# Kernel optimization log

Hardware: AMD Instinct MI355X
Metric: run time of the kernel (lower is better)

The kernel has to match this reference:

```python
import jax, jax.numpy as jnp
import numpy as np

N = 128
MAX_LEN = 1024
L = 1024
BATCH = 32


def _legs_transition(n):
    # HiPPO-LegS A, B matrices (float64 numpy, matches torch module's transition())
    q = np.arange(n, dtype=np.float64)
    col, row = np.meshgrid(q, q)
    r = 2 * q + 1
    M = -(np.where(row >= col, r, 0) - np.diag(q))
    T = np.sqrt(np.diag(2 * q + 1))
    A = T @ M @ np.linalg.inv(T)
    B = np.diag(T)
    return A, B


def _stacked_bilinear(n, max_length):
    # Bilinear discretization per timestep t: (I - A/(2t))^{-1} (I + A/(2t)), (I - A/(2t))^{-1} B/t
    A, B = _legs_transition(n)
    t = np.arange(1, max_length + 1, dtype=np.float64)[:, None, None]  # (L,1,1)
    I = np.eye(n)
    At = A[None] / t                                   # (L,N,N)
    lhs = I - At / 2
    A_st = np.linalg.solve(lhs, I + At / 2)            # (L,N,N)
    Bt = (B[None, :] / t[:, 0, 0][:, None])[..., None]  # (L,N,1)
    B_st = np.linalg.solve(lhs, Bt)[..., 0]            # (L,N)
    return A_st.astype(np.float32), B_st.astype(np.float32)


def setup_inputs() -> dict:
    key = jax.random.key(0)
    inputs = jax.random.normal(key, (L, BATCH), dtype=jnp.float32)
    A_st, B_st = _stacked_bilinear(N, MAX_LEN)
    return {
        "inputs": inputs,
        "A_stacked": jnp.asarray(A_st),
        "B_stacked": jnp.asarray(B_st),
    }


def reference(inputs, A_stacked, B_stacked):
    # inputs: (L, B); A_stacked: (L, N, N); B_stacked: (L, N)
    Lc = inputs.shape[0]
    u = inputs[..., None] * B_stacked[:Lc, None, :]  # (L, B, N)

    def step(s, Au):
        A_t, u_t = Au                                 # (N,N), (B,N)
        s = jnp.einsum("ij,bj->bi", A_t, s) + u_t
        return s, s

    s0 = jnp.zeros_like(u[0])
    _, xs = jax.lax.scan(step, s0, (A_stacked[:Lc], u))
    return xs  # (L, B, N)
```

## Files before the change

kernel.cpp:

```cpp
#include <hip/hip_runtime.h>


#define LDK 136
#define PKF 11264

using f16 = _Float16;
typedef __attribute__((ext_vector_type(8))) f16 f16x8;
typedef __attribute__((ext_vector_type(4))) float f32x4;

__device__ __forceinline__ f32x4 mfma3(f16x8 ah, f16x8 al, f16x8 bh, f16x8 bl,
                                       f32x4 c) {
  c = __builtin_amdgcn_mfma_f32_16x16x32_f16(ah, bh, c, 0, 0, 0);
  c = __builtin_amdgcn_mfma_f32_16x16x32_f16(ah, bl, c, 0, 0, 0);
  c = __builtin_amdgcn_mfma_f32_16x16x32_f16(al, bh, c, 0, 0, 0);
  return c;
}

__device__ __forceinline__ void split8(const float* v, f16x8& h, f16x8& l) {
#pragma unroll
  for (int j = 0; j < 8; ++j) {
    const float x = v[j];
    const f16 hh = (f16)x;
    h[j] = hh;
    l[j] = (f16)(x - (float)hh);
  }
}

__device__ __forceinline__ int slot2mt(int h, int slot) {
  if (h == 0) return (slot & 1) ? 7 - (slot >> 1) : (slot >> 1);
  return (slot & 1) ? 5 - (slot >> 1) : 2 + (slot >> 1);
}

__device__ __forceinline__ void gload_lds16(const float* g, float* l) {
  __builtin_amdgcn_global_load_lds(
      (const __attribute__((address_space(1))) unsigned int*)g,
      (__attribute__((address_space(3))) unsigned int*)l, 16, 0, 0);
}


__device__ __forceinline__ int pk_src_off(int m) {
  int b, local, ccm1, sh;
  if (m < 128)      { b = 0; local = m;       ccm1 = 3;  sh = 2; }
  else if (m < 384) { b = 1; local = m - 128; ccm1 = 7;  sh = 3; }
  else if (m < 896) { b = 2; local = m - 384; ccm1 = 15; sh = 4; }
  else              { b = 3; local = m - 896; ccm1 = 15; sh = 4; }
  const int ri = local >> sh, cp = local & ccm1;
  const int c = cp ^ (ri & ccm1);
  return (b * 32 + ri) * 128 + c * 8;
}

__device__ __forceinline__ void read_pk(const f16* __restrict__ Bs, int nt,
                                        int lr, int j0, f16x8& v) {
  const int b = nt >> 1;
  const int ri = ((nt & 1) << 4) + lr;
  const int ccm1 = (b == 0) ? 3 : (b == 1) ? 7 : 15;
  const int fb = (b == 0) ? 0 : (b == 1) ? 1024 : (b == 2) ? 3072 : 7168;
  const int c = j0 ^ (ri & ccm1);
  v = *(const f16x8*)(Bs + fb + ri * ((ccm1 + 1) * 8) + c * 8);
}

template <int NT, int IT>
__device__ __forceinline__ void pk_precompute(int tid, int (&src)[IT]) {
#pragma unroll
  for (int it = 0; it < IT; ++it) {
    const int m = tid + it * NT;
    src[it] = (m < 1408) ? pk_src_off(m) : 0;
  }
}

template <int NT, int IT>
__device__ __forceinline__ void pk_stage(const f16* __restrict__ gMh,
                                         const f16* __restrict__ gMl,
                                         f16* __restrict__ dH,
                                         f16* __restrict__ dL,
                                         const int (&src)[IT], int tid) {
#pragma unroll
  for (int it = 0; it < IT; ++it) {
    const int m = tid + it * NT;
    if (it < IT - 1 || m < 1408) {
      gload_lds16((const float*)(gMh + src[it]), (float*)(dH + m * 8));
      gload_lds16((const float*)(gMl + src[it]), (float*)(dL + m * 8));
    }
  }
}

__device__ __forceinline__ void compute_soff(int tid, int (&soff)[8]) {
#pragma unroll
  for (int it = 0; it < 8; ++it) {
    const int m = tid + it * 320;
    if (m < 2304) {
      const int kt = (m >= 768) + (m >= 1536) + (m >= 2048);
      const int local = m - ((kt >= 1) * 768 + (kt >= 2) * 768 + (kt >= 3) * 512);
      const int rp = local >> 3, c = local & 7;
      const int r = rp + 32 + (kt >= 2) * 32 + (kt >= 3) * 32;
      soff[it] = r * 128 + kt * 32 + ((c ^ (rp & 7)) << 2);
    } else {
      soff[it] = 0;
    }
  }
}

__device__ __forceinline__ void issue_A(const float* __restrict__ Al,
                                        float* __restrict__ Ast,
                                        const int (&soff)[8], int tid) {
#pragma unroll
  for (int it = 0; it < 8; ++it) {
    if (it < 7 || tid < 64)
      gload_lds16(Al + soff[it], Ast + (tid + it * 320) * 4);
  }
}

__device__ __forceinline__ void read_staged(const float* __restrict__ Ast,
                                            int nt, int kt, int lr, int q,
                                            f16x8& ch, f16x8& cl) {
  const int rp = nt * 16 + lr - (32 + (kt >= 2) * 32 + (kt >= 3) * 32);
  const float* pb =
      Ast + ((kt >= 1) * 3072 + (kt >= 2) * 3072 + (kt >= 3) * 2048) + rp * 32;
  float raw[8];
  *(float4*)&raw[0] = *(const float4*)(pb + (((2 * q + 0) ^ (rp & 7)) << 2));
  *(float4*)&raw[4] = *(const float4*)(pb + (((2 * q + 1) ^ (rp & 7)) << 2));
  split8(raw, ch, cl);
}

__device__ __forceinline__ void chain_step_pk(
    const f16* __restrict__ Bsh, const f16* __restrict__ Bsl,
    const float* __restrict__ aux0, f16* __restrict__ Ph, f16* __restrict__ Pl,
    int wv, int mt, const f16* __restrict__ nMh, const f16* __restrict__ nMl,
    f16* __restrict__ stH, f16* __restrict__ stL, const int (&src)[5],
    int tid) {
  const int lane = tid & 63;
  const int lr = lane & 15, q = lane >> 4;
  const bool wrow = (mt >= 8);
  const int ktA0 = wrow ? 0 : (mt >> 1);
  f16x8 ah[4], al[4];
#pragma unroll
  for (int kt = 0; kt < 4; ++kt) {
    if (kt >= ktA0) {
      const int off = (wv * 16 + lr) * LDK + kt * 32 + q * 8;
      ah[kt] = *(const f16x8*)(Ph + off);
      al[kt] = *(const f16x8*)(Pl + off);
    }
  }
  f32x4 acc[8];
#pragma unroll
  for (int nt = 0; nt < 8; ++nt) acc[nt] = (f32x4){0.f, 0.f, 0.f, 0.f};
#pragma unroll
  for (int nt = 0; nt < 8; ++nt) {
    if (wrow || nt >= mt) {
#pragma unroll
      for (int kt = 0; kt < 4; ++kt) {
        if (kt >= ktA0 && kt <= (nt >> 1)) {
          f16x8 bh, bl;
          const int j0 = kt * 4 + q;
          read_pk(Bsh, nt, lr, j0, bh);
          read_pk(Bsl, nt, lr, j0, bl);
          acc[nt] = mfma3(ah[kt], al[kt], bh, bl, acc[nt]);
        }
      }
    }
  }
  __syncthreads();
  if (nMh) pk_stage<320, 5>(nMh, nMl, stH, stL, src, tid);
#pragma unroll
  for (int nt = 0; nt < 8; ++nt) {
    if (!(wrow || nt >= mt)) continue;
    float v[4] = {acc[nt][0], acc[nt][1], acc[nt][2], acc[nt][3]};
    if (wrow) {
      const int b0 = (mt - 8) * 16 + q * 4;
      const float4 w4 = *(const float4*)(aux0 + (nt * 16 + lr) * 32 + b0);
      v[0] += w4.x; v[1] += w4.y; v[2] += w4.z; v[3] += w4.w;
    }
#pragma unroll
    for (int r = 0; r < 4; ++r) {
      const int o = (wv * 16 + q * 4 + r) * LDK + nt * 16 + lr;
      const f16 hh = (f16)v[r];
      Ph[o] = hh;
      Pl[o] = (f16)(v[r] - (float)hh);
    }
  }
  __syncthreads();
}

__device__ __forceinline__ void chain_step_k1(const float* __restrict__ Acur,
                                              const float* __restrict__ Anext,
                                              const float* __restrict__ x32,
                                              const float* __restrict__ Bvl,
                                              f16* __restrict__ Ph,
                                              f16* __restrict__ Pl,
                                              float* __restrict__ Ast,
                                              const int (&soff)[8],
                                              int wv, int mt) {
  const int tid = threadIdx.x;
  const int lane = tid & 63, lr = lane & 15, q = lane >> 4;
  const bool wrow = (mt >= 8);
  const int ktA0 = wrow ? 0 : (mt >> 1);
  f16x8 ah[4], al[4];
#pragma unroll
  for (int kt = 0; kt < 4; ++kt) {
    if (kt >= ktA0) {
      const int off = (wv * 16 + lr) * LDK + kt * 32 + q * 8;
      ah[kt] = *(const f16x8*)(Ph + off);
      al[kt] = *(const f16x8*)(Pl + off);
    }
  }
  const bool need0 = wrow || mt == 0;
  const bool need1 = wrow || mt <= 1;
  float dir0[8], dir1[8];
  if (need0) {
    const float* p = Acur + lr * 128 + q * 8;
    *(float4*)&dir0[0] = *(const float4*)p;
    *(float4*)&dir0[4] = *(const float4*)(p + 4);
  }
  if (need1) {
    const float* p = Acur + (16 + lr) * 128 + q * 8;
    *(float4*)&dir1[0] = *(const float4*)p;
    *(float4*)&dir1[4] = *(const float4*)(p + 4);
  }
  f32x4 acc[8];
#pragma unroll
  for (int nt = 0; nt < 8; ++nt) acc[nt] = (f32x4){0.f, 0.f, 0.f, 0.f};
#pragma unroll
  for (int nt = 2; nt < 8; ++nt) {
    if (wrow || nt >= mt) {
#pragma unroll
      for (int kt = 0; kt < 4; ++kt) {
        if (kt >= ktA0 && kt <= (nt >> 1)) {
          f16x8 ch, cl;
          read_staged(Ast, nt, kt, lr, q, ch, cl);
          acc[nt] = mfma3(ah[kt], al[kt], ch, cl, acc[nt]);
        }
      }
    }
  }
  if (need0) {
    f16x8 ch, cl;
    split8(dir0, ch, cl);
    acc[0] = mfma3(ah[0], al[0], ch, cl, acc[0]);
  }
  if (need1) {
    f16x8 ch, cl;
    split8(dir1, ch, cl);
    acc[1] = mfma3(ah[0], al[0], ch, cl, acc[1]);
  }
  __syncthreads();
  if (Anext) issue_A(Anext, Ast, soff, tid);
#pragma unroll
  for (int nt = 0; nt < 8; ++nt) {
    if (!(wrow || nt >= mt)) continue;
    float v[4] = {acc[nt][0], acc[nt][1], acc[nt][2], acc[nt][3]};
    if (wrow) {
      const int b0 = (mt - 8) * 16 + q * 4;
      const float4 x4 = *(const float4*)(x32 + b0);
      const float bn = Bvl[nt * 16 + lr];
      v[0] += bn * x4.x; v[1] += bn * x4.y; v[2] += bn * x4.z; v[3] += bn * x4.w;
    }
#pragma unroll
    for (int r = 0; r < 4; ++r) {
      const int o = (wv * 16 + q * 4 + r) * LDK + nt * 16 + lr;
      const f16 hh = (f16)v[r];
      Ph[o] = hh;
      Pl[o] = (f16)(v[r] - (float)hh);
    }
  }
  __syncthreads();
}

__device__ __forceinline__ void chain_copyout(const f16* __restrict__ Ph,
                                              const f16* __restrict__ Pl, int h,
                                              f16* __restrict__ oMh,
                                              f16* __restrict__ oMl,
                                              float* __restrict__ oW) {
  const int tid = threadIdx.x;
  for (int t = tid; t < 1024; t += 320) {
    const int i = t >> 3;
    const int slot = (t >> 1) & 3;
    const int half = t & 1;
    const int mtg = slot2mt(h, slot);
    const int y0 = mtg * 16 + half * 8;
    if ((y0 >> 5) > (i >> 5)) continue;
    f16x8 hv, lv;
#pragma unroll
    for (int e = 0; e < 8; ++e) {
      hv[e] = Ph[(slot * 16 + half * 8 + e) * LDK + i];
      lv[e] = Pl[(slot * 16 + half * 8 + e) * LDK + i];
    }
    *(f16x8*)(oMh + i * 128 + y0) = hv;
    *(f16x8*)(oMl + i * 128 + y0) = lv;
  }
  for (int t = tid; t < 512; t += 320) {
    const int n = t >> 2, b4 = (t & 3) * 4;
    float4 o;
    float* po = (float*)&o;
#pragma unroll
    for (int e = 0; e < 4; ++e)
      po[e] = (float)Ph[(64 + b4 + e) * LDK + n] + (float)Pl[(64 + b4 + e) * LDK + n];
    *(float4*)(oW + n * 32 + h * 16 + b4) = o;
  }
}

__device__ __forceinline__ void load_prev_to_P(const f16* pMh, const f16* pMl,
                                               const float* pW, int h,
                                               f16* Ph, f16* Pl) {
  const int tid = threadIdx.x;
  for (int t = tid; t < 1024; t += 320) {
    const int k = t >> 3, u = t & 7;
    const int slot = u >> 1, half = u & 1;
    const int mtg = slot2mt(h, slot);
    const int y0 = mtg * 16 + half * 8;
    f16x8 hv, lv;
    if ((y0 >> 5) <= (k >> 5)) {
      hv = *(const f16x8*)(pMh + k * 128 + y0);
      lv = *(const f16x8*)(pMl + k * 128 + y0);
    } else {
#pragma unroll
      for (int e = 0; e < 8; ++e) { hv[e] = (f16)0.f; lv[e] = (f16)0.f; }
    }
#pragma unroll
    for (int e = 0; e < 8; ++e) {
      Ph[(slot * 16 + half * 8 + e) * LDK + k] = hv[e];
      Pl[(slot * 16 + half * 8 + e) * LDK + k] = lv[e];
    }
  }
  for (int t = tid; t < 2048; t += 320) {
    const int n = t >> 4, b = t & 15;
    const float wv0 = pW[n * 32 + h * 16 + b];
    const f16 hh = (f16)wv0;
    Ph[(64 + b) * LDK + n] = hh;
    Pl[(64 + b) * LDK + n] = (f16)(wv0 - (float)hh);
  }
  __syncthreads();
}

__device__ __forceinline__ void state_step_h_b16(const f16* __restrict__ Bh16,
                                                 const f16* __restrict__ Bl16,
                                                 const float* __restrict__ aux0,
                                                 f16* __restrict__ Sh,
                                                 f16* __restrict__ Sl, int h) {
  const int tid = threadIdx.x;
  const int wv4 = tid >> 6;
  const bool act = (wv4 < 4);
  const int wv = wv4 & 3;
  const int lane = tid & 63, lr = lane & 15, q = lane >> 4;
  const int nts[2] = {wv, 7 - wv};
  const int ktAmax = (7 - wv) >> 1;
  f16x8 ah[4], al[4];
  f16x8 bh[2][4], bl[2][4];
  f32x4 acc[2];
  if (act) {
#pragma unroll
    for (int kt = 0; kt < 4; ++kt)
      if (kt <= ktAmax) {
        const int off = lr * LDK + kt * 32 + q * 8;
        ah[kt] = *(const f16x8*)(Sh + off);
        al[kt] = *(const f16x8*)(Sl + off);
      }
#pragma unroll
    for (int ni = 0; ni < 2; ++ni) {
      const int nt = nts[ni];
#pragma unroll
      for (int kt = 0; kt < 4; ++kt)
        if (kt <= (nt >> 1)) {
          const int o = (nt * 16 + lr) * 128 + kt * 32 + q * 8;
          bh[ni][kt] = *(const f16x8*)(Bh16 + o);
          bl[ni][kt] = *(const f16x8*)(Bl16 + o);
        }
    }
#pragma unroll
    for (int ni = 0; ni < 2; ++ni) acc[ni] = (f32x4){0.f, 0.f, 0.f, 0.f};
#pragma unroll
    for (int ni = 0; ni < 2; ++ni) {
      const int nt = nts[ni];
#pragma unroll
      for (int kt = 0; kt < 4; ++kt)
        if (kt <= (nt >> 1))
          acc[ni] = mfma3(ah[kt], al[kt], bh[ni][kt], bl[ni][kt], acc[ni]);
    }
  }
  __syncthreads();
  if (act) {
#pragma unroll
    for (int ni = 0; ni < 2; ++ni) {
      const int nt = nts[ni];
      float v[4] = {acc[ni][0], acc[ni][1], acc[ni][2], acc[ni][3]};
      const int bq = q * 4;
      const float4 w4 = *(const float4*)(aux0 + (nt * 16 + lr) * 32 + h * 16 + bq);
      v[0] += w4.x; v[1] += w4.y; v[2] += w4.z; v[3] += w4.w;
#pragma unroll
      for (int r = 0; r < 4; ++r) {
        const int o = (bq + r) * LDK + nt * 16 + lr;
        const f16 hh = (f16)v[r];
        Sh[o] = hh;
        Sl[o] = (f16)(v[r] - (float)hh);
      }
    }
  }
  __syncthreads();
}

__device__ __forceinline__ void state_step_pk(
    const f16* __restrict__ Bsh, const f16* __restrict__ Bsl,
    const float* __restrict__ aux0, f16* __restrict__ Sh,
    f16* __restrict__ Sl, int h, const f16* __restrict__ nMh,
    const f16* __restrict__ nMl, f16* __restrict__ stH,
    f16* __restrict__ stL, const int (&src)[6], int tid) {
  const int wv = (tid >> 6) & 3;
  const int lane = tid & 63, lr = lane & 15, q = lane >> 4;
  const int nts[2] = {wv, 7 - wv};
  const int ktAmax = (7 - wv) >> 1;
  f16x8 ah[4], al[4];
#pragma unroll
  for (int kt = 0; kt < 4; ++kt)
    if (kt <= ktAmax) {
      const int off = lr * LDK + kt * 32 + q * 8;
      ah[kt] = *(const f16x8*)(Sh + off);
      al[kt] = *(const f16x8*)(Sl + off);
    }
  f32x4 acc[2];
#pragma unroll
  for (int ni = 0; ni < 2; ++ni) acc[ni] = (f32x4){0.f, 0.f, 0.f, 0.f};
#pragma unroll
  for (int ni = 0; ni < 2; ++ni) {
    const int nt = nts[ni];
#pragma unroll
    for (int kt = 0; kt < 4; ++kt)
      if (kt <= (nt >> 1)) {
        f16x8 bh, bl;
        const int j0 = kt * 4 + q;
        read_pk(Bsh, nt, lr, j0, bh);
        read_pk(Bsl, nt, lr, j0, bl);
        acc[ni] = mfma3(ah[kt], al[kt], bh, bl, acc[ni]);
      }
  }
  __syncthreads();
  if (nMh) pk_stage<256, 6>(nMh, nMl, stH, stL, src, tid);
#pragma unroll
  for (int ni = 0; ni < 2; ++ni) {
    const int nt = nts[ni];
    float v[4] = {acc[ni][0], acc[ni][1], acc[ni][2], acc[ni][3]};
    const int bq = q * 4;
    const float4 w4 = *(const float4*)(aux0 + (nt * 16 + lr) * 32 + h * 16 + bq);
    v[0] += w4.x; v[1] += w4.y; v[2] += w4.z; v[3] += w4.w;
#pragma unroll
    for (int r = 0; r < 4; ++r) {
      const int o = (bq + r) * LDK + nt * 16 + lr;
      const f16 hh = (f16)v[r];
      Sh[o] = hh;
      Sl[o] = (f16)(v[r] - (float)hh);
    }
  }
  __syncthreads();
}

__device__ __forceinline__ void state_step_h_staged(
    const float* __restrict__ Acur, const float* __restrict__ Anext,
    const float* __restrict__ x32, const float* __restrict__ Bvl,
    f16* __restrict__ Sh, f16* __restrict__ Sl, float* __restrict__ outp,
    int h, float* __restrict__ Ast, const int (&soff)[8]) {
  const int tid = threadIdx.x;
  const int wv4 = tid >> 6;
  const bool act = (wv4 < 4);
  const int wv = wv4 & 3;
  const int lane = tid & 63, lr = lane & 15, q = lane >> 4;
  const int ntL = wv, ntH = 7 - wv;
  f32x4 accL = (f32x4){0.f, 0.f, 0.f, 0.f}, accH = accL;
  if (act) {
    const int ktAmax = ntH >> 1;
    f16x8 ah[4], al[4];
#pragma unroll
    for (int kt = 0; kt < 4; ++kt)
      if (kt <= ktAmax) {
        const int off = lr * LDK + kt * 32 + q * 8;
        ah[kt] = *(const f16x8*)(Sh + off);
        al[kt] = *(const f16x8*)(Sl + off);
      }
    float dir[8];
    if (wv < 2) {
      const float* p = Acur + (ntL * 16 + lr) * 128 + q * 8;
      *(float4*)&dir[0] = *(const float4*)p;
      *(float4*)&dir[4] = *(const float4*)(p + 4);
    }
#pragma unroll
    for (int kt = 0; kt < 4; ++kt) {
      if (kt <= (ntH >> 1)) {
        f16x8 ch, cl;
        read_staged(Ast, ntH, kt, lr, q, ch, cl);
        accH = mfma3(ah[kt], al[kt], ch, cl, accH);
      }
    }
    if (wv >= 2) {
#pragma unroll
      for (int kt = 0; kt < 4; ++kt) {
        if (kt <= (ntL >> 1)) {
          f16x8 ch, cl;
          read_staged(Ast, ntL, kt, lr, q, ch, cl);
          accL = mfma3(ah[kt], al[kt], ch, cl, accL);
        }
      }
    } else {
      f16x8 ch, cl;
      split8(dir, ch, cl);
      accL = mfma3(ah[0], al[0], ch, cl, accL);
    }
  }
  __syncthreads();
  if (Anext) issue_A(Anext, Ast, soff, tid);
  if (act) {
#pragma unroll
    for (int ni = 0; ni < 2; ++ni) {
      const int nt = (ni == 0) ? ntL : ntH;
      const f32x4 a = (ni == 0) ? accL : accH;
      float v[4] = {a[0], a[1], a[2], a[3]};
      const int bq = q * 4;
      const float4 x4 = *(const float4*)(x32 + h * 16 + bq);
      const float bn = Bvl[nt * 16 + lr];
      v[0] += bn * x4.x; v[1] += bn * x4.y; v[2] += bn * x4.z; v[3] += bn * x4.w;
      if (outp) {
#pragma unroll
        for (int r = 0; r < 4; ++r)
          outp[(h * 16 + bq + r) * 128 + nt * 16 + lr] = v[r];
      }
#pragma unroll
      for (int r = 0; r < 4; ++r) {
        const int o = (bq + r) * LDK + nt * 16 + lr;
        const f16 hh = (f16)v[r];
        Sh[o] = hh;
        Sl[o] = (f16)(v[r] - (float)hh);
      }
    }
  }
  __syncthreads();
}

__global__ __launch_bounds__(320) void k1_chunks(const float* __restrict__ A,
                                                 const float* __restrict__ x,
                                                 const float* __restrict__ Bv,
                                                 f16* __restrict__ Mh,
                                                 f16* __restrict__ Ml,
                                                 float* __restrict__ Wf) {
  __shared__ f16 Ph[80 * LDK], Pl[80 * LDK];
  __shared__ float Ast[9216];
  const int tid = threadIdx.x;
  const int c = blockIdx.x >> 1, h = blockIdx.x & 1;
  const int l0 = 4 * c;
  int soff[8];
  compute_soff(tid, soff);
  issue_A(A + (size_t)(l0 + 1) * 16384, Ast, soff, tid);
  const float* A0 = A + (size_t)l0 * 16384;
  for (int t = tid; t < 2048; t += 320) {
    const int k = t >> 4, u = t & 15;
    const int slot = u >> 2, fo = (u & 3) * 4;
    const int mtg = slot2mt(h, slot);
    const int y = mtg * 16 + fo;
    float vv[4];
    if ((y >> 5) <= (k >> 5)) {
      const float4 v = *(const float4*)(A0 + k * 128 + y);
      vv[0] = v.x; vv[1] = v.y; vv[2] = v.z; vv[3] = v.w;
    } else {
      vv[0] = vv[1] = vv[2] = vv[3] = 0.f;
    }
#pragma unroll
    for (int e = 0; e < 4; ++e) {
      const f16 hh = (f16)vv[e];
      Ph[(slot * 16 + fo + e) * LDK + k] = hh;
      Pl[(slot * 16 + fo + e) * LDK + k] = (f16)(vv[e] - (float)hh);
    }
  }
  for (int t = tid; t < 512; t += 320) {
    const int b = t >> 5, n4 = (t & 31) * 4;
    const float xb = x[l0 * 32 + h * 16 + b];
#pragma unroll
    for (int e = 0; e < 4; ++e) {
      const float u = xb * Bv[l0 * 128 + n4 + e];
      const f16 hh = (f16)u;
      Ph[(64 + b) * LDK + n4 + e] = hh;
      Pl[(64 + b) * LDK + n4 + e] = (f16)(u - (float)hh);
    }
  }
  __syncthreads();
  const int wv = tid >> 6;
  const int mt = (wv == 4) ? (8 + h) : slot2mt(h, wv);
  chain_step_k1(A + (size_t)(l0 + 1) * 16384, A + (size_t)(l0 + 2) * 16384,
                x + (l0 + 1) * 32, Bv + (l0 + 1) * 128, Ph, Pl, Ast, soff, wv, mt);
  chain_step_k1(A + (size_t)(l0 + 2) * 16384, A + (size_t)(l0 + 3) * 16384,
                x + (l0 + 2) * 32, Bv + (l0 + 2) * 128, Ph, Pl, Ast, soff, wv, mt);
  chain_step_k1(A + (size_t)(l0 + 3) * 16384, nullptr,
                x + (l0 + 3) * 32, Bv + (l0 + 3) * 128, Ph, Pl, Ast, soff, wv, mt);
  chain_copyout(Ph, Pl, h, Mh + (size_t)c * 16384, Ml + (size_t)c * 16384,
                Wf + (size_t)c * 4096);
}

__global__ __launch_bounds__(320) void mscan(const f16* __restrict__ MhA,
                                             const f16* __restrict__ MlA,
                                             const float* __restrict__ WA,
                                             f16* __restrict__ MhB,
                                             f16* __restrict__ MlB,
                                             float* __restrict__ WB) {
  __shared__ f16 Ph[80 * LDK], Pl[80 * LDK];
  __shared__ f16 BstH[2][PKF], BstL[2][PKF];
  const int g = blockIdx.x >> 1, h = blockIdx.x & 1;
  const int tid = threadIdx.x;
  int src[5];
  pk_precompute<320, 5>(tid, src);
  const size_t n0 = (size_t)(16 * g);
  pk_stage<320, 5>(MhA + (n0 + 1) * 16384, MlA + (n0 + 1) * 16384,
                   BstH[1], BstL[1], src, tid);
  load_prev_to_P(MhA + n0 * 16384, MlA + n0 * 16384, WA + n0 * 4096, h, Ph, Pl);
  const int wv = tid >> 6;
  const int mt = (wv == 4) ? (8 + h) : slot2mt(h, wv);
#pragma unroll 1
  for (int j = 1; j <= 15; ++j) {
    const size_t nd = n0 + j;
    const int cur = j & 1;
    const bool more = (j < 15);
    chain_step_pk(BstH[cur], BstL[cur], WA + nd * 4096, Ph, Pl, wv, mt,
                  more ? MhA + (nd + 1) * 16384 : nullptr,
                  more ? MlA + (nd + 1) * 16384 : nullptr,
                  BstH[cur ^ 1], BstL[cur ^ 1], src, tid);
    chain_copyout(Ph, Pl, h, MhB + nd * 16384, MlB + nd * 16384,
                  WB + nd * 4096);
  }
}

__global__ __launch_bounds__(256) void gscan(const f16* __restrict__ MhB,
                                             const f16* __restrict__ MlB,
                                             const float* __restrict__ WB,
                                             float* __restrict__ Ef) {
  __shared__ f16 Sh[16 * LDK], Sl[16 * LDK];
  __shared__ f16 GstH[2][PKF], GstL[2][PKF];
  const int g = blockIdx.x >> 1, h = blockIdx.x & 1;
  const int tid = threadIdx.x;
  int src[6];
  pk_precompute<256, 6>(tid, src);
  for (int t = tid; t < 16 * LDK; t += 256) { Sh[t] = (f16)0.f; Sl[t] = (f16)0.f; }
  if (g > 0)
    pk_stage<256, 6>(MhB + (size_t)15 * 16384, MlB + (size_t)15 * 16384,
                     GstH[0], GstL[0], src, tid);
  __syncthreads();
#pragma unroll 1
  for (int t = 0; t < g; ++t) {
    const size_t nd = (size_t)(16 * t + 15);
    const size_t nn = (size_t)(16 * (t + 1) + 15);
    const int cur = t & 1;
    const bool more = (t + 1 < g);
    state_step_pk(GstH[cur], GstL[cur], WB + nd * 4096, Sh, Sl, h,
                  more ? MhB + nn * 16384 : nullptr,
                  more ? MlB + nn * 16384 : nullptr,
                  GstH[cur ^ 1], GstL[cur ^ 1], src, tid);
  }
  for (int t = tid; t < 2048; t += 256) {
    const int row = t & 15, n = t >> 4;
    Ef[(size_t)g * 4096 + n * 32 + h * 16 + row] =
        (float)Sh[row * LDK + n] + (float)Sl[row * LDK + n];
  }
}

__global__ __launch_bounds__(320) void k3h(const float* __restrict__ A,
                                           const float* __restrict__ x,
                                           const float* __restrict__ Bv,
                                           const f16* __restrict__ MhA,
                                           const f16* __restrict__ MlA,
                                           const float* __restrict__ WA,
                                           const f16* __restrict__ MhB,
                                           const f16* __restrict__ MlB,
                                           const float* __restrict__ WB,
                                           const float* __restrict__ Ef,
                                           float* __restrict__ out) {
  __shared__ f16 Sh[16 * LDK], Sl[16 * LDK];
  __shared__ float Ast[9216];
  const int tid = threadIdx.x;
  const int c = blockIdx.x >> 1, h = blockIdx.x & 1;
  const int g = c >> 4, j = c & 15;
  int soff[8];
  compute_soff(tid, soff);
  issue_A(A + (size_t)(4 * c) * 16384, Ast, soff, tid);
  const float* Ew = Ef + (size_t)g * 4096;
  for (int tt = tid; tt < 2048; tt += 320) {
    const int row = tt & 15, n = tt >> 4;
    const float v = Ew[n * 32 + h * 16 + row];
    const f16 hh = (f16)v;
    Sh[row * LDK + n] = hh;
    Sl[row * LDK + n] = (f16)(v - (float)hh);
  }
  __syncthreads();
  if (j > 0) {
    const int nd = c - 1, jp = j - 1;
    const bool inA = (jp == 0);
    const f16* mh = (inA ? MhA : MhB) + (size_t)nd * 16384;
    const f16* ml = (inA ? MlA : MlB) + (size_t)nd * 16384;
    const float* w = (inA ? WA : WB) + (size_t)nd * 4096;
    state_step_h_b16(mh, ml, w, Sh, Sl, h);
  }
#pragma unroll 1
  for (int t4 = 0; t4 < 4; ++t4) {
    const int l = 4 * c + t4;
    const float* Anext = (t4 < 3) ? A + (size_t)(l + 1) * 16384 : nullptr;
    state_step_h_staged(A + (size_t)l * 16384, Anext, x + l * 32, Bv + l * 128,
                        Sh, Sl, out + (size_t)l * 4096, h, Ast, soff);
  }
}

extern "C" void kernel_launch(void* const* d_in, const int* in_sizes, int n_in,
                              void* d_out, int out_size, void* d_ws, size_t ws_size,
                              hipStream_t stream) {
  const float* x  = (const float*)d_in[0];
  const float* A  = (const float*)d_in[1];
  const float* Bv = (const float*)d_in[2];
  float* out = (float*)d_out;

  f16* MhA = (f16*)d_ws;
  f16* MlA = MhA + 256 * 16384;
  float* WA = (float*)(MlA + 256 * 16384);
  f16* MhB = (f16*)(WA + 256 * 4096);
  f16* MlB = MhB + 256 * 16384;
  float* WB = (float*)(MlB + 256 * 16384);
  float* Ef = WB + 256 * 4096;

  k1_chunks<<<512, 320, 0, stream>>>(A, x, Bv, MhA, MlA, WA);
  mscan<<<32, 320, 0, stream>>>(MhA, MlA, WA, MhB, MlB, WB);
  gscan<<<32, 256, 0, stream>>>(MhB, MlB, WB, Ef);
  k3h<<<512, 320, 0, stream>>>(A, x, Bv, MhA, MlA, WA, MhB, MlB, WB, Ef, out);
}
```

Before: 292.2 us.

## Split mscan work across twice as many smaller blocks and write outputs directly

The chunk-prefix matrix scan kernel now runs as 64 blocks of 192 threads instead of 32 blocks of 320. Each block handles half of the row slots, and only one half-block carries the W row. Results are written straight from accumulators to global memory, which drops the separate copy-out pass and one barrier per step. Prefetch staging is issued at the start of each step in both mscan and gscan rather than after a mid-step barrier. This spreads a serial, latency-bound phase over more CUs, at the cost of loading the shared B staging matrices twice and leaving some waves idle.

```diff
diff --git a/kernel.cpp b/kernel.cpp
--- a/kernel.cpp
+++ b/kernel.cpp
@@ -6,6 +6,7 @@
 
 using f16 = _Float16;
 typedef __attribute__((ext_vector_type(8))) f16 f16x8;
+typedef __attribute__((ext_vector_type(4))) f16 f16x4;
 typedef __attribute__((ext_vector_type(4))) float f32x4;
 
 __device__ __forceinline__ f32x4 mfma3(f16x8 ah, f16x8 al, f16x8 bh, f16x8 bl,
@@ -77,7 +78,7 @@
 #pragma unroll
   for (int it = 0; it < IT; ++it) {
     const int m = tid + it * NT;
-    if (it < IT - 1 || m < 1408) {
+    if (m < 1408) {
       gload_lds16((const float*)(gMh + src[it]), (float*)(dH + m * 8));
       gload_lds16((const float*)(gMl + src[it]), (float*)(dL + m * 8));
     }
@@ -120,65 +121,6 @@
   *(float4*)&raw[0] = *(const float4*)(pb + (((2 * q + 0) ^ (rp & 7)) << 2));
   *(float4*)&raw[4] = *(const float4*)(pb + (((2 * q + 1) ^ (rp & 7)) << 2));
   split8(raw, ch, cl);
-}
-
-__device__ __forceinline__ void chain_step_pk(
-    const f16* __restrict__ Bsh, const f16* __restrict__ Bsl,
-    const float* __restrict__ aux0, f16* __restrict__ Ph, f16* __restrict__ Pl,
-    int wv, int mt, const f16* __restrict__ nMh, const f16* __restrict__ nMl,
-    f16* __restrict__ stH, f16* __restrict__ stL, const int (&src)[5],
-    int tid) {
-  const int lane = tid & 63;
-  const int lr = lane & 15, q = lane >> 4;
-  const bool wrow = (mt >= 8);
-  const int ktA0 = wrow ? 0 : (mt >> 1);
-  f16x8 ah[4], al[4];
-#pragma unroll
-  for (int kt = 0; kt < 4; ++kt) {
-    if (kt >= ktA0) {
-      const int off = (wv * 16 + lr) * LDK + kt * 32 + q * 8;
-      ah[kt] = *(const f16x8*)(Ph + off);
-      al[kt] = *(const f16x8*)(Pl + off);
-    }
-  }
-  f32x4 acc[8];
-#pragma unroll
-  for (int nt = 0; nt < 8; ++nt) acc[nt] = (f32x4){0.f, 0.f, 0.f, 0.f};
-#pragma unroll
-  for (int nt = 0; nt < 8; ++nt) {
-    if (wrow || nt >= mt) {
-#pragma unroll
-      for (int kt = 0; kt < 4; ++kt) {
-        if (kt >= ktA0 && kt <= (nt >> 1)) {
-          f16x8 bh, bl;
-          const int j0 = kt * 4 + q;
-          read_pk(Bsh, nt, lr, j0, bh);
-          read_pk(Bsl, nt, lr, j0, bl);
-          acc[nt] = mfma3(ah[kt], al[kt], bh, bl, acc[nt]);
-        }
-      }
-    }
-  }
-  __syncthreads();
-  if (nMh) pk_stage<320, 5>(nMh, nMl, stH, stL, src, tid);
-#pragma unroll
-  for (int nt = 0; nt < 8; ++nt) {
-    if (!(wrow || nt >= mt)) continue;
-    float v[4] = {acc[nt][0], acc[nt][1], acc[nt][2], acc[nt][3]};
-    if (wrow) {
-      const int b0 = (mt - 8) * 16 + q * 4;
-      const float4 w4 = *(const float4*)(aux0 + (nt * 16 + lr) * 32 + b0);
-      v[0] += w4.x; v[1] += w4.y; v[2] += w4.z; v[3] += w4.w;
-    }
-#pragma unroll
-    for (int r = 0; r < 4; ++r) {
-      const int o = (wv * 16 + q * 4 + r) * LDK + nt * 16 + lr;
-      const f16 hh = (f16)v[r];
-      Ph[o] = hh;
-      Pl[o] = (f16)(v[r] - (float)hh);
-    }
-  }
-  __syncthreads();
 }
 
 __device__ __forceinline__ void chain_step_k1(const float* __restrict__ Acur,
@@ -296,39 +238,6 @@
       po[e] = (float)Ph[(64 + b4 + e) * LDK + n] + (float)Pl[(64 + b4 + e) * LDK + n];
     *(float4*)(oW + n * 32 + h * 16 + b4) = o;
   }
-}
-
-__device__ __forceinline__ void load_prev_to_P(const f16* pMh, const f16* pMl,
-                                               const float* pW, int h,
-                                               f16* Ph, f16* Pl) {
-  const int tid = threadIdx.x;
-  for (int t = tid; t < 1024; t += 320) {
-    const int k = t >> 3, u = t & 7;
-    const int slot = u >> 1, half = u & 1;
-    const int mtg = slot2mt(h, slot);
-    const int y0 = mtg * 16 + half * 8;
-    f16x8 hv, lv;
-    if ((y0 >> 5) <= (k >> 5)) {
-      hv = *(const f16x8*)(pMh + k * 128 + y0);
-      lv = *(const f16x8*)(pMl + k * 128 + y0);
-    } else {
-#pragma unroll
-      for (int e = 0; e < 8; ++e) { hv[e] = (f16)0.f; lv[e] = (f16)0.f; }
-    }
-#pragma unroll
-    for (int e = 0; e < 8; ++e) {
-      Ph[(slot * 16 + half * 8 + e) * LDK + k] = hv[e];
-      Pl[(slot * 16 + half * 8 + e) * LDK + k] = lv[e];
-    }
-  }
-  for (int t = tid; t < 2048; t += 320) {
-    const int n = t >> 4, b = t & 15;
-    const float wv0 = pW[n * 32 + h * 16 + b];
-    const f16 hh = (f16)wv0;
-    Ph[(64 + b) * LDK + n] = hh;
-    Pl[(64 + b) * LDK + n] = (f16)(wv0 - (float)hh);
-  }
-  __syncthreads();
 }
 
 __device__ __forceinline__ void state_step_h_b16(const f16* __restrict__ Bh16,
@@ -392,60 +301,6 @@
         Sh[o] = hh;
         Sl[o] = (f16)(v[r] - (float)hh);
       }
-    }
-  }
-  __syncthreads();
-}
-
-__device__ __forceinline__ void state_step_pk(
-    const f16* __restrict__ Bsh, const f16* __restrict__ Bsl,
-    const float* __restrict__ aux0, f16* __restrict__ Sh,
-    f16* __restrict__ Sl, int h, const f16* __restrict__ nMh,
-    const f16* __restrict__ nMl, f16* __restrict__ stH,
-    f16* __restrict__ stL, const int (&src)[6], int tid) {
-  const int wv = (tid >> 6) & 3;
-  const int lane = tid & 63, lr = lane & 15, q = lane >> 4;
-  const int nts[2] = {wv, 7 - wv};
-  const int ktAmax = (7 - wv) >> 1;
-  f16x8 ah[4], al[4];
-#pragma unroll
-  for (int kt = 0; kt < 4; ++kt)
-    if (kt <= ktAmax) {
-      const int off = lr * LDK + kt * 32 + q * 8;
-      ah[kt] = *(const f16x8*)(Sh + off);
-      al[kt] = *(const f16x8*)(Sl + off);
-    }
-  f32x4 acc[2];
-#pragma unroll
-  for (int ni = 0; ni < 2; ++ni) acc[ni] = (f32x4){0.f, 0.f, 0.f, 0.f};
-#pragma unroll
-  for (int ni = 0; ni < 2; ++ni) {
-    const int nt = nts[ni];
-#pragma unroll
-    for (int kt = 0; kt < 4; ++kt)
-      if (kt <= (nt >> 1)) {
-        f16x8 bh, bl;
-        const int j0 = kt * 4 + q;
-        read_pk(Bsh, nt, lr, j0, bh);
-        read_pk(Bsl, nt, lr, j0, bl);
-        acc[ni] = mfma3(ah[kt], al[kt], bh, bl, acc[ni]);
-      }
-  }
-  __syncthreads();
-  if (nMh) pk_stage<256, 6>(nMh, nMl, stH, stL, src, tid);
-#pragma unroll
-  for (int ni = 0; ni < 2; ++ni) {
-    const int nt = nts[ni];
-    float v[4] = {acc[ni][0], acc[ni][1], acc[ni][2], acc[ni][3]};
-    const int bq = q * 4;
-    const float4 w4 = *(const float4*)(aux0 + (nt * 16 + lr) * 32 + h * 16 + bq);
-    v[0] += w4.x; v[1] += w4.y; v[2] += w4.z; v[3] += w4.w;
-#pragma unroll
-    for (int r = 0; r < 4; ++r) {
-      const int o = (bq + r) * LDK + nt * 16 + lr;
-      const f16 hh = (f16)v[r];
-      Sh[o] = hh;
-      Sl[o] = (f16)(v[r] - (float)hh);
     }
   }
   __syncthreads();
@@ -589,35 +444,161 @@
                 Wf + (size_t)c * 4096);
 }
 
-__global__ __launch_bounds__(320) void mscan(const f16* __restrict__ MhA,
-                                             const f16* __restrict__ MlA,
-                                             const float* __restrict__ WA,
-                                             f16* __restrict__ MhB,
-                                             f16* __restrict__ MlB,
-                                             float* __restrict__ WB) {
-  __shared__ f16 Ph[80 * LDK], Pl[80 * LDK];
+__global__ __launch_bounds__(192) void mscan_s(const f16* __restrict__ MhA,
+                                               const f16* __restrict__ MlA,
+                                               const float* __restrict__ WA,
+                                               f16* __restrict__ MhB,
+                                               f16* __restrict__ MlB,
+                                               float* __restrict__ WB) {
+  __shared__ f16 Ph[48 * LDK], Pl[48 * LDK];
   __shared__ f16 BstH[2][PKF], BstL[2][PKF];
-  const int g = blockIdx.x >> 1, h = blockIdx.x & 1;
+  const int bid = blockIdx.x;
+  const int g = bid >> 2, h = (bid >> 1) & 1, half = bid & 1;
   const int tid = threadIdx.x;
-  int src[5];
-  pk_precompute<320, 5>(tid, src);
+  const int wv = tid >> 6;
+  const int lane = tid & 63, lr = lane & 15, q = lane >> 4;
+  const bool isW = (half == 0 && wv == 2);
+  const bool isM = (wv < 2);
+  const int mt = isW ? (8 + h) : (isM ? slot2mt(h, half * 2 + wv) : 0);
+  const int lw = wv * 16;
+  const int ktA0 = isW ? 0 : (mt >> 1);
   const size_t n0 = (size_t)(16 * g);
-  pk_stage<320, 5>(MhA + (n0 + 1) * 16384, MlA + (n0 + 1) * 16384,
+
+  int src[8];
+  pk_precompute<192, 8>(tid, src);
+  pk_stage<192, 8>(MhA + (n0 + 1) * 16384, MlA + (n0 + 1) * 16384,
                    BstH[1], BstL[1], src, tid);
-  load_prev_to_P(MhA + n0 * 16384, MlA + n0 * 16384, WA + n0 * 4096, h, Ph, Pl);
-  const int wv = tid >> 6;
-  const int mt = (wv == 4) ? (8 + h) : slot2mt(h, wv);
+  if (isM) {
+    const f16* pMh = MhA + n0 * 16384;
+    const f16* pMl = MlA + n0 * 16384;
+#pragma unroll
+    for (int it = 0; it < 4; ++it) {
+      const int t = lane + it * 64;
+      const int k = t >> 1, hk = t & 1;
+      const int y0 = mt * 16 + hk * 8;
+      f16x8 hv, lv;
+      if ((y0 >> 5) <= (k >> 5)) {
+        hv = *(const f16x8*)(pMh + k * 128 + y0);
+        lv = *(const f16x8*)(pMl + k * 128 + y0);
+      } else {
+#pragma unroll
+        for (int e = 0; e < 8; ++e) { hv[e] = (f16)0.f; lv[e] = (f16)0.f; }
+      }
+#pragma unroll
+      for (int e = 0; e < 8; ++e) {
+        Ph[(lw + hk * 8 + e) * LDK + k] = hv[e];
+        Pl[(lw + hk * 8 + e) * LDK + k] = lv[e];
+      }
+    }
+  } else if (isW) {
+    const float* pW = WA + n0 * 4096;
+#pragma unroll
+    for (int it = 0; it < 8; ++it) {
+      const int t = lane + it * 64;
+      const int n = t >> 2, b4 = (t & 3) * 4;
+      const float4 w4 = *(const float4*)(pW + n * 32 + h * 16 + b4);
+      const float vv[4] = {w4.x, w4.y, w4.z, w4.w};
+#pragma unroll
+      for (int r = 0; r < 4; ++r) {
+        const f16 hh = (f16)vv[r];
+        Ph[(lw + b4 + r) * LDK + n] = hh;
+        Pl[(lw + b4 + r) * LDK + n] = (f16)(vv[r] - (float)hh);
+      }
+    }
+  }
+  __syncthreads();
+
 #pragma unroll 1
   for (int j = 1; j <= 15; ++j) {
     const size_t nd = n0 + j;
     const int cur = j & 1;
-    const bool more = (j < 15);
-    chain_step_pk(BstH[cur], BstL[cur], WA + nd * 4096, Ph, Pl, wv, mt,
-                  more ? MhA + (nd + 1) * 16384 : nullptr,
-                  more ? MlA + (nd + 1) * 16384 : nullptr,
-                  BstH[cur ^ 1], BstL[cur ^ 1], src, tid);
-    chain_copyout(Ph, Pl, h, MhB + nd * 16384, MlB + nd * 16384,
-                  WB + nd * 4096);
+    if (j < 15)
+      pk_stage<192, 8>(MhA + (nd + 1) * 16384, MlA + (nd + 1) * 16384,
+                       BstH[cur ^ 1], BstL[cur ^ 1], src, tid);
+    float4 w4s[8];
+    if (isW) {
+      const float* Wn = WA + nd * 4096;
+#pragma unroll
+      for (int nt = 0; nt < 8; ++nt)
+        w4s[nt] = *(const float4*)(Wn + (nt * 16 + lr) * 32 + h * 16 + q * 4);
+    }
+    f16x8 ah[4], al[4];
+    if (isM || isW) {
+#pragma unroll
+      for (int kt = 0; kt < 4; ++kt)
+        if (kt >= ktA0) {
+          const int off = (lw + lr) * LDK + kt * 32 + q * 8;
+          ah[kt] = *(const f16x8*)(Ph + off);
+          al[kt] = *(const f16x8*)(Pl + off);
+        }
+    }
+    f32x4 acc[8];
+#pragma unroll
+    for (int nt = 0; nt < 8; ++nt) acc[nt] = (f32x4){0.f, 0.f, 0.f, 0.f};
+    if (isM || isW) {
+      const int ntF = isW ? 0 : mt;
+#pragma unroll
+      for (int nt = 0; nt < 8; ++nt) {
+        if (nt >= ntF) {
+#pragma unroll
+          for (int kt = 0; kt < 4; ++kt) {
+            if (kt >= ktA0 && kt <= (nt >> 1)) {
+              f16x8 bh, bl;
+              const int j0 = kt * 4 + q;
+              read_pk(BstH[cur], nt, lr, j0, bh);
+              read_pk(BstL[cur], nt, lr, j0, bl);
+              acc[nt] = mfma3(ah[kt], al[kt], bh, bl, acc[nt]);
+            }
+          }
+        }
+      }
+    }
+    if (isM) {
+      f16* oMh = MhB + nd * 16384;
+      f16* oMl = MlB + nd * 16384;
+      if (mt & 1) {
+        const int k = (mt - 1) * 16 + lr;
+        const f16x4 z = {(f16)0.f, (f16)0.f, (f16)0.f, (f16)0.f};
+        *(f16x4*)(oMh + k * 128 + mt * 16 + q * 4) = z;
+        *(f16x4*)(oMl + k * 128 + mt * 16 + q * 4) = z;
+      }
+#pragma unroll
+      for (int nt = 0; nt < 8; ++nt) {
+        if (nt < mt) continue;
+        f16x4 hv4, lv4;
+#pragma unroll
+        for (int r = 0; r < 4; ++r) {
+          const float v = acc[nt][r];
+          const f16 hh = (f16)v;
+          const f16 ll = (f16)(v - (float)hh);
+          hv4[r] = hh;
+          lv4[r] = ll;
+          Ph[(lw + q * 4 + r) * LDK + nt * 16 + lr] = hh;
+          Pl[(lw + q * 4 + r) * LDK + nt * 16 + lr] = ll;
+        }
+        const int k = nt * 16 + lr;
+        *(f16x4*)(oMh + k * 128 + mt * 16 + q * 4) = hv4;
+        *(f16x4*)(oMl + k * 128 + mt * 16 + q * 4) = lv4;
+      }
+    } else if (isW) {
+      float* oW = WB + nd * 4096;
+#pragma unroll
+      for (int nt = 0; nt < 8; ++nt) {
+        float v[4];
+#pragma unroll
+        for (int r = 0; r < 4; ++r) v[r] = acc[nt][r];
+        v[0] += w4s[nt].x; v[1] += w4s[nt].y; v[2] += w4s[nt].z; v[3] += w4s[nt].w;
+#pragma unroll
+        for (int r = 0; r < 4; ++r) {
+          const f16 hh = (f16)v[r];
+          Ph[(lw + q * 4 + r) * LDK + nt * 16 + lr] = hh;
+          Pl[(lw + q * 4 + r) * LDK + nt * 16 + lr] = (f16)(v[r] - (float)hh);
+        }
+        const float4 o = {v[0], v[1], v[2], v[3]};
+        *(float4*)(oW + (nt * 16 + lr) * 32 + h * 16 + q * 4) = o;
+      }
+    }
+    __syncthreads();
   }
 }
 
@@ -636,16 +617,63 @@
     pk_stage<256, 6>(MhB + (size_t)15 * 16384, MlB + (size_t)15 * 16384,
                      GstH[0], GstL[0], src, tid);
   __syncthreads();
+  const int wv = (tid >> 6) & 3;
+  const int lane = tid & 63, lr = lane & 15, q = lane >> 4;
+  const int nts[2] = {wv, 7 - wv};
+  const int ktAmax = (7 - wv) >> 1;
 #pragma unroll 1
   for (int t = 0; t < g; ++t) {
     const size_t nd = (size_t)(16 * t + 15);
-    const size_t nn = (size_t)(16 * (t + 1) + 15);
     const int cur = t & 1;
-    const bool more = (t + 1 < g);
-    state_step_pk(GstH[cur], GstL[cur], WB + nd * 4096, Sh, Sl, h,
-                  more ? MhB + nn * 16384 : nullptr,
-                  more ? MlB + nn * 16384 : nullptr,
-                  GstH[cur ^ 1], GstL[cur ^ 1], src, tid);
+    if (t + 1 < g) {
+      const size_t nn = (size_t)(16 * (t + 1) + 15);
+      pk_stage<256, 6>(MhB + nn * 16384, MlB + nn * 16384,
+                       GstH[cur ^ 1], GstL[cur ^ 1], src, tid);
+    }
+    const float* aux0 = WB + nd * 4096;
+    float4 w4s[2];
+#pragma unroll
+    for (int ni = 0; ni < 2; ++ni)
+      w4s[ni] = *(const float4*)(aux0 + (nts[ni] * 16 + lr) * 32 + h * 16 + q * 4);
+    f16x8 ah[4], al[4];
+#pragma unroll
+    for (int kt = 0; kt < 4; ++kt)
+      if (kt <= ktAmax) {
+        const int off = lr * LDK + kt * 32 + q * 8;
+        ah[kt] = *(const f16x8*)(Sh + off);
+        al[kt] = *(const f16x8*)(Sl + off);
+      }
+    f32x4 acc[2];
+#pragma unroll
+    for (int ni = 0; ni < 2; ++ni) acc[ni] = (f32x4){0.f, 0.f, 0.f, 0.f};
+#pragma unroll
+    for (int ni = 0; ni < 2; ++ni) {
+      const int nt = nts[ni];
+#pragma unroll
+      for (int kt = 0; kt < 4; ++kt)
+        if (kt <= (nt >> 1)) {
+          f16x8 bh, bl;
+          const int j0 = kt * 4 + q;
+          read_pk(GstH[cur], nt, lr, j0, bh);
+          read_pk(GstL[cur], nt, lr, j0, bl);
+          acc[ni] = mfma3(ah[kt], al[kt], bh, bl, acc[ni]);
+        }
+    }
+    __syncthreads();
+#pragma unroll
+    for (int ni = 0; ni < 2; ++ni) {
+      const int nt = nts[ni];
+      float v[4] = {acc[ni][0], acc[ni][1], acc[ni][2], acc[ni][3]};
+      v[0] += w4s[ni].x; v[1] += w4s[ni].y; v[2] += w4s[ni].z; v[3] += w4s[ni].w;
+#pragma unroll
+      for (int r = 0; r < 4; ++r) {
+        const int o = (q * 4 + r) * LDK + nt * 16 + lr;
+        const f16 hh = (f16)v[r];
+        Sh[o] = hh;
+        Sl[o] = (f16)(v[r] - (float)hh);
+      }
+    }
+    __syncthreads();
   }
   for (int t = tid; t < 2048; t += 256) {
     const int row = t & 15, n = t >> 4;
@@ -716,7 +744,7 @@
   float* Ef = WB + 256 * 4096;
 
   k1_chunks<<<512, 320, 0, stream>>>(A, x, Bv, MhA, MlA, WA);
-  mscan<<<32, 320, 0, stream>>>(MhA, MlA, WA, MhB, MlB, WB);
+  mscan_s<<<64, 192, 0, stream>>>(MhA, MlA, WA, MhB, MlB, WB);
   gscan<<<32, 256, 0, stream>>>(MhB, MlB, WB, Ef);
   k3h<<<512, 320, 0, stream>>>(A, x, Bv, MhA, MlA, WA, MhB, MlB, WB, Ef, out);
 }
```

Result: faster. 252.8 us (-13.5%).
